# Performance work log

Hardware: AMD Instinct MI355X
Metric: run time of the kernel (lower is better)

## Reference

```python
import jax, jax.numpy as jnp
import numpy as np

FEAT = 1024
DEPTH = 3
NUM_SCALES = 5
N_NODES = 2 ** DEPTH - 1  # 7
N_LEAVES = 2 ** DEPTH     # 8
HID = 64
LN_EPS = 1e-5


def setup_inputs() -> dict:
    key = jax.random.key(0)
    ks = jax.random.split(key, 16)
    B, D = 8192, 4096
    s = 0.02
    return {
        "features": jax.random.normal(ks[0], (B, FEAT), jnp.float32),
        "logits": jax.random.normal(ks[1], (NUM_SCALES, B, D), jnp.float32),
        # all 7 tree nodes stacked (identical shapes at every level)
        "tw1": jax.random.normal(ks[2], (N_NODES, HID, FEAT), jnp.float32) * s,
        "tb1": jnp.zeros((N_NODES, HID), jnp.float32),
        "tg": jnp.ones((N_NODES, HID), jnp.float32),   # LayerNorm gamma
        "tbn": jnp.zeros((N_NODES, HID), jnp.float32),  # LayerNorm beta
        "tw2": jax.random.normal(ks[3], (N_NODES, 2, HID), jnp.float32) * s,
        "tb2": jnp.zeros((N_NODES, 2), jnp.float32),
        # leaf_to_scale: Linear(8, 10) -> GELU -> Linear(10, 5)
        "lw1": jax.random.normal(ks[4], (NUM_SCALES * 2, N_LEAVES), jnp.float32) * s,
        "lb1": jnp.zeros((NUM_SCALES * 2,), jnp.float32),
        "lw2": jax.random.normal(ks[5], (NUM_SCALES, NUM_SCALES * 2), jnp.float32) * s,
        "lb2": jnp.zeros((NUM_SCALES,), jnp.float32),
        # direct_gate: Linear(1024, 256) -> GELU -> Linear(256, 5)
        "dw1": jax.random.normal(ks[6], (FEAT // 4, FEAT), jnp.float32) * s,
        "db1": jnp.zeros((FEAT // 4,), jnp.float32),
        "dw2": jax.random.normal(ks[7], (NUM_SCALES, FEAT // 4), jnp.float32) * s,
        "db2": jnp.zeros((NUM_SCALES,), jnp.float32),
        "combine_weight": jnp.asarray(0.7, jnp.float32),
    }


def _forward(features, logits, tw1, tb1, tg, tbn, tw2, tb2,
             lw1, lb1, lw2, lb2, dw1, db1, dw2, db2, combine_weight):
    B = features.shape[0]
    # all tree nodes in one batched GEMM: [B, 7, 64]
    h = jnp.einsum("bf,nhf->bnh", features, tw1) + tb1
    mu = jnp.mean(h, axis=-1, keepdims=True)
    var = jnp.var(h, axis=-1, keepdims=True)
    h = (h - mu) / jnp.sqrt(var + LN_EPS) * tg + tbn
    h = jax.nn.gelu(h, approximate=False)  # torch GELU default = exact
    node_logits = jnp.einsum("bnh,noh->bno", h, tw2) + tb2  # [B, 7, 2]
    node_probs = jax.nn.softmax(node_logits / 0.5, axis=-1)
    # traverse levels: node ordering is BFS (level 0: node 0, level 1: 1..2, level 2: 3..6)
    p = jnp.ones((B, 1), features.dtype)
    offset = 0
    for level in range(DEPTH):
        n = 2 ** level
        pr = node_probs[:, offset:offset + n]          # [B, n, 2]
        p = (p[:, :, None] * pr).reshape(B, 2 * n)      # children interleaved L,R
        offset += n
    leaf_probs = p  # [B, 8]
    t = jax.nn.gelu(leaf_probs @ lw1.T + lb1, approximate=False)
    tree_gates = jax.nn.softmax(t @ lw2.T + lb2, axis=-1)
    d = jax.nn.gelu(features @ dw1.T + db1, approximate=False)
    direct_gates = jax.nn.softmax(d @ dw2.T + db2, axis=-1)
    w = jax.nn.sigmoid(combine_weight)
    gates = w * tree_gates + (1.0 - w) * direct_gates
    gates = gates / jnp.sum(gates, axis=-1, keepdims=True)
    # weighted combine over scales: memory-bound reduction over 5 large tensors
    combined = jnp.einsum("bs,sbd->bd", gates, logits)
    return combined, gates


def reference(features, logits, tw1, tb1, tg, tbn, tw2, tb2,
              lw1, lb1, lw2, lb2, dw1, db1, dw2, db2, combine_weight):
    return _forward(features, logits, tw1, tb1, tg, tbn, tw2, tb2,
                    lw1, lb1, lw2, lb2, dw1, db1, dw2, db2, combine_weight)
```

## Files before the change

kernel.cpp:

```cpp
#include <hip/hip_runtime.h>
#include <math.h>

#define B_SZ   8192
#define FEATN  1024
#define DCOL   4096
#define NS     5
#define NN     7
#define HIDN   64
#define NTREE  448
#define NDIR   256
#define NTOT   704

#define BM 128
#define BN 64
#define BK 16
#define LDA 132
#define LDB 68

__global__ __launch_bounds__(256) void htg_gemm(
    const float* __restrict__ A, const float* __restrict__ tw1,
    const float* __restrict__ dw1, float* __restrict__ hidden)
{
    __shared__ float As[BK * LDA];
    __shared__ float Bs[BK * LDB];
    const int tid = threadIdx.x;
    const int bm0 = blockIdx.x * BM;
    const int bn0 = blockIdx.y * BN;
    const float* Wsrc = (bn0 < NTREE) ? (tw1 + (size_t)bn0 * FEATN)
                                      : (dw1 + (size_t)(bn0 - NTREE) * FEATN);
    const int ty  = tid >> 4;
    const int tx  = tid & 15;
    const int lr  = tid >> 2;
    const int lc4 = tid & 3;

    float acc[8][4];
#pragma unroll
    for (int i = 0; i < 8; ++i)
#pragma unroll
        for (int j = 0; j < 4; ++j) acc[i][j] = 0.f;

    float4 aR0, aR1, bR;
    {
        const float* Ap = A + (size_t)(bm0 + lr) * FEATN + lc4 * 4;
        aR0 = *(const float4*)(Ap);
        aR1 = *(const float4*)(Ap + (size_t)64 * FEATN);
        bR  = *(const float4*)(Wsrc + (size_t)lr * FEATN + lc4 * 4);
    }
    const int KT = FEATN / BK;
    for (int kt = 0; kt < KT; ++kt) {
        {
            float av0[4] = {aR0.x, aR0.y, aR0.z, aR0.w};
            float av1[4] = {aR1.x, aR1.y, aR1.z, aR1.w};
            float bv[4]  = {bR.x,  bR.y,  bR.z,  bR.w};
#pragma unroll
            for (int j = 0; j < 4; ++j) {
                As[(lc4 * 4 + j) * LDA + lr]      = av0[j];
                As[(lc4 * 4 + j) * LDA + lr + 64] = av1[j];
                Bs[(lc4 * 4 + j) * LDB + lr]      = bv[j];
            }
        }
        __syncthreads();
        if (kt + 1 < KT) {
            const int k0 = (kt + 1) * BK;
            const float* Ap = A + (size_t)(bm0 + lr) * FEATN + k0 + lc4 * 4;
            aR0 = *(const float4*)(Ap);
            aR1 = *(const float4*)(Ap + (size_t)64 * FEATN);
            bR  = *(const float4*)(Wsrc + (size_t)lr * FEATN + k0 + lc4 * 4);
        }
#pragma unroll
        for (int kk = 0; kk < BK; ++kk) {
            float4 a0 = *(const float4*)&As[kk * LDA + ty * 8];
            float4 a1 = *(const float4*)&As[kk * LDA + ty * 8 + 4];
            float4 b  = *(const float4*)&Bs[kk * LDB + tx * 4];
            float av[8] = {a0.x, a0.y, a0.z, a0.w, a1.x, a1.y, a1.z, a1.w};
            float bv[4] = {b.x, b.y, b.z, b.w};
#pragma unroll
            for (int i = 0; i < 8; ++i)
#pragma unroll
                for (int j = 0; j < 4; ++j)
                    acc[i][j] = fmaf(av[i], bv[j], acc[i][j]);
        }
        __syncthreads();
    }
#pragma unroll
    for (int i = 0; i < 8; ++i) {
        const int row = bm0 + ty * 8 + i;
        float4 v = make_float4(acc[i][0], acc[i][1], acc[i][2], acc[i][3]);
        *(float4*)&hidden[(size_t)row * NTOT + bn0 + tx * 4] = v;
    }
}

__device__ inline float wredsum(float v) {
#pragma unroll
    for (int o = 32; o > 0; o >>= 1) v += __shfl_xor(v, o, 64);
    return v;
}
__device__ inline float gelu_exact(float x) {
    return 0.5f * x * (1.f + erff(x * 0.70710678118654752f));
}
__device__ inline void softmax5(float* v) {
    float m = v[0];
#pragma unroll
    for (int s = 1; s < NS; ++s) m = fmaxf(m, v[s]);
    float sum = 0.f;
#pragma unroll
    for (int s = 0; s < NS; ++s) { v[s] = expf(v[s] - m); sum += v[s]; }
    float inv = 1.f / sum;
#pragma unroll
    for (int s = 0; s < NS; ++s) v[s] *= inv;
}

__global__ __launch_bounds__(64) void htg_gates(
    const float* __restrict__ hidden,
    const float* __restrict__ tb1, const float* __restrict__ tg,
    const float* __restrict__ tbn, const float* __restrict__ tw2,
    const float* __restrict__ tb2,
    const float* __restrict__ lw1, const float* __restrict__ lb1,
    const float* __restrict__ lw2, const float* __restrict__ lb2,
    const float* __restrict__ db1, const float* __restrict__ dw2,
    const float* __restrict__ db2, const float* __restrict__ cw,
    float* __restrict__ gates_out)
{
    const int b = blockIdx.x;
    const int l = threadIdx.x;
    const float* hb = hidden + (size_t)b * NTOT;

    float np0[NN], np1[NN];
#pragma unroll
    for (int n = 0; n < NN; ++n) {
        float x  = hb[n * 64 + l] + tb1[n * 64 + l];
        float s  = wredsum(x);
        float sq = wredsum(x * x);
        float mu  = s * (1.f / 64.f);
        float var = sq * (1.f / 64.f) - mu * mu;
        float xn  = (x - mu) * rsqrtf(var + 1e-5f);
        xn = xn * tg[n * 64 + l] + tbn[n * 64 + l];
        float g = gelu_exact(xn);
        float o0 = wredsum(g * tw2[(n * 2 + 0) * 64 + l]) + tb2[n * 2 + 0];
        float o1 = wredsum(g * tw2[(n * 2 + 1) * 64 + l]) + tb2[n * 2 + 1];
        float p0 = 1.f / (1.f + expf(2.f * (o1 - o0)));
        np0[n] = p0; np1[n] = 1.f - p0;
    }
    float lp[8];
#pragma unroll
    for (int leaf = 0; leaf < 8; ++leaf) {
        const int c0 = (leaf >> 2) & 1, c1 = (leaf >> 1) & 1, c2 = leaf & 1;
        float v0 = c0 ? np1[0] : np0[0];
        float v1 = c1 ? np1[1 + c0] : np0[1 + c0];
        float v2 = c2 ? np1[3 + 2 * c0 + c1] : np0[3 + 2 * c0 + c1];
        lp[leaf] = v0 * v1 * v2;
    }
    float t[10];
#pragma unroll
    for (int j = 0; j < 10; ++j) {
        float a = lb1[j];
#pragma unroll
        for (int leaf = 0; leaf < 8; ++leaf) a = fmaf(lp[leaf], lw1[j * 8 + leaf], a);
        t[j] = gelu_exact(a);
    }
    float tgt[NS];
#pragma unroll
    for (int s = 0; s < NS; ++s) {
        float a = lb2[s];
#pragma unroll
        for (int j = 0; j < 10; ++j) a = fmaf(t[j], lw2[s * 10 + j], a);
        tgt[s] = a;
    }
    softmax5(tgt);

    float dacc[NS] = {0.f, 0.f, 0.f, 0.f, 0.f};
#pragma unroll
    for (int i = 0; i < 4; ++i) {
        const int j = i * 64 + l;
        float d = gelu_exact(hb[NTREE + j] + db1[j]);
#pragma unroll
        for (int s = 0; s < NS; ++s) dacc[s] = fmaf(d, dw2[s * 256 + j], dacc[s]);
    }
    float dgt[NS];
#pragma unroll
    for (int s = 0; s < NS; ++s) dgt[s] = wredsum(dacc[s]) + db2[s];
    softmax5(dgt);

    const float w = 1.f / (1.f + expf(-cw[0]));
    float g5[NS]; float sum = 0.f;
#pragma unroll
    for (int s = 0; s < NS; ++s) { g5[s] = w * tgt[s] + (1.f - w) * dgt[s]; sum += g5[s]; }
    float inv = 1.f / sum;
    if (l < NS) gates_out[(size_t)b * NS + l] = g5[l] * inv;
}

__global__ __launch_bounds__(256) void htg_combine(
    const float* __restrict__ logits, const float* __restrict__ gates,
    float* __restrict__ out)
{
    const int b  = blockIdx.x >> 2;
    const int d4 = ((blockIdx.x & 3) << 8) + threadIdx.x;
    float g[NS];
#pragma unroll
    for (int s = 0; s < NS; ++s) g[s] = gates[(size_t)b * NS + s];
    const float4* lp = (const float4*)logits;
    const size_t base = (size_t)b * (DCOL / 4) + d4;
    float4 a = make_float4(0.f, 0.f, 0.f, 0.f);
#pragma unroll
    for (int s = 0; s < NS; ++s) {
        float4 v = lp[(size_t)s * B_SZ * (DCOL / 4) + base];
        a.x = fmaf(g[s], v.x, a.x);
        a.y = fmaf(g[s], v.y, a.y);
        a.z = fmaf(g[s], v.z, a.z);
        a.w = fmaf(g[s], v.w, a.w);
    }
    ((float4*)out)[base] = a;
}

extern "C" void kernel_launch(void* const* d_in, const int* in_sizes, int n_in,
                              void* d_out, int out_size, void* d_ws, size_t ws_size,
                              hipStream_t stream) {
    const float* features = (const float*)d_in[0];
    const float* logits   = (const float*)d_in[1];
    const float* tw1      = (const float*)d_in[2];
    const float* tb1      = (const float*)d_in[3];
    const float* tg       = (const float*)d_in[4];
    const float* tbn      = (const float*)d_in[5];
    const float* tw2      = (const float*)d_in[6];
    const float* tb2      = (const float*)d_in[7];
    const float* lw1      = (const float*)d_in[8];
    const float* lb1      = (const float*)d_in[9];
    const float* lw2      = (const float*)d_in[10];
    const float* lb2      = (const float*)d_in[11];
    const float* dw1      = (const float*)d_in[12];
    const float* db1      = (const float*)d_in[13];
    const float* dw2      = (const float*)d_in[14];
    const float* db2      = (const float*)d_in[15];
    const float* cw       = (const float*)d_in[16];

    float* out = (float*)d_out;
    float* gates = out + (size_t)B_SZ * DCOL;

    const size_t hidden_bytes = (size_t)B_SZ * NTOT * sizeof(float);
    float* hidden = (ws_size >= hidden_bytes) ? (float*)d_ws : (float*)d_out;

    dim3 gemm_grid(B_SZ / BM, NTOT / BN);
    htg_gemm<<<gemm_grid, 256, 0, stream>>>(features, tw1, dw1, hidden);

    htg_gates<<<B_SZ, 64, 0, stream>>>(hidden, tb1, tg, tbn, tw2, tb2,
                                       lw1, lb1, lw2, lb2, db1, dw2, db2, cw,
                                       gates);

    htg_combine<<<B_SZ * 4, 256, 0, stream>>>(logits, gates, out);
}
```

Measured before the change: 1.095 ms.

## Fuse LayerNorm/GELU/node heads into GEMM epilogue and slim gate kernel

The GEMM epilogue now applies bias, LayerNorm, exact GELU and the two-output node head per 64-column tile. For the direct branch it applies GELU and partial dot products with dw2. Only 7 node probabilities and 20 partial sums per row are written, instead of the full 704-wide hidden matrix. The gate kernel becomes one thread per row reading that small scratch. The combine kernel handles one row per block with nontemporal loads and stores. This removes a large intermediate round trip and the per-row wave reductions, at the cost of more epilogue work and register pressure in the GEMM.

```diff
diff --git a/kernel.cpp b/kernel.cpp
--- a/kernel.cpp
+++ b/kernel.cpp
@@ -11,15 +11,27 @@
 #define NDIR   256
 #define NTOT   704
 
+
 #define BM 128
 #define BN 64
 #define BK 16
 #define LDA 132
 #define LDB 68
 
-__global__ __launch_bounds__(256) void htg_gemm(
+typedef float f32x4_t __attribute__((ext_vector_type(4)));
+
+__device__ inline float gelu_exact(float x) {
+    return 0.5f * x * (1.f + erff(x * 0.70710678118654752f));
+}
+
+__global__ __launch_bounds__(256) void htg_gemm_fused(
     const float* __restrict__ A, const float* __restrict__ tw1,
-    const float* __restrict__ dw1, float* __restrict__ hidden)
+    const float* __restrict__ dw1,
+    const float* __restrict__ tb1, const float* __restrict__ tg,
+    const float* __restrict__ tbn, const float* __restrict__ tw2,
+    const float* __restrict__ tb2,
+    const float* __restrict__ db1, const float* __restrict__ dw2,
+    float* __restrict__ np_out, float* __restrict__ dpart_out)
 {
     __shared__ float As[BK * LDA];
     __shared__ float Bs[BK * LDB];
@@ -82,22 +94,89 @@
         }
         __syncthreads();
     }
-#pragma unroll
-    for (int i = 0; i < 8; ++i) {
-        const int row = bm0 + ty * 8 + i;
-        float4 v = make_float4(acc[i][0], acc[i][1], acc[i][2], acc[i][3]);
-        *(float4*)&hidden[(size_t)row * NTOT + bn0 + tx * 4] = v;
-    }
-}
-
-__device__ inline float wredsum(float v) {
-#pragma unroll
-    for (int o = 32; o > 0; o >>= 1) v += __shfl_xor(v, o, 64);
-    return v;
-}
-__device__ inline float gelu_exact(float x) {
-    return 0.5f * x * (1.f + erff(x * 0.70710678118654752f));
-}
+
+    const int ib = blockIdx.y;
+    if (ib < NN) {
+        const int n = ib;
+        const int col = tx * 4;
+        const float4 tb1v = *(const float4*)&tb1[n * HIDN + col];
+        const float4 tgv  = *(const float4*)&tg [n * HIDN + col];
+        const float4 tbnv = *(const float4*)&tbn[n * HIDN + col];
+        const float4 w2av = *(const float4*)&tw2[(n * 2 + 0) * HIDN + col];
+        const float4 w2bv = *(const float4*)&tw2[(n * 2 + 1) * HIDN + col];
+        const float b2a = tb2[n * 2], b2b = tb2[n * 2 + 1];
+        const float tb1a[4] = {tb1v.x, tb1v.y, tb1v.z, tb1v.w};
+        const float tga[4]  = {tgv.x,  tgv.y,  tgv.z,  tgv.w};
+        const float tbna[4] = {tbnv.x, tbnv.y, tbnv.z, tbnv.w};
+        const float w2aa[4] = {w2av.x, w2av.y, w2av.z, w2av.w};
+        const float w2ba[4] = {w2bv.x, w2bv.y, w2bv.z, w2bv.w};
+#pragma unroll
+        for (int i = 0; i < 8; ++i) {
+            float x[4]; float s = 0.f, sq = 0.f;
+#pragma unroll
+            for (int j = 0; j < 4; ++j) {
+                x[j] = acc[i][j] + tb1a[j];
+                s += x[j];
+                sq = fmaf(x[j], x[j], sq);
+            }
+#pragma unroll
+            for (int o = 8; o > 0; o >>= 1) {
+                s  += __shfl_xor(s,  o, 64);
+                sq += __shfl_xor(sq, o, 64);
+            }
+            const float mu  = s * (1.f / 64.f);
+            const float var = sq * (1.f / 64.f) - mu * mu;
+            const float rs  = rsqrtf(var + 1e-5f);
+            float o0 = 0.f, o1 = 0.f;
+#pragma unroll
+            for (int j = 0; j < 4; ++j) {
+                const float g = gelu_exact((x[j] - mu) * rs * tga[j] + tbna[j]);
+                o0 = fmaf(g, w2aa[j], o0);
+                o1 = fmaf(g, w2ba[j], o1);
+            }
+#pragma unroll
+            for (int o = 8; o > 0; o >>= 1) {
+                o0 += __shfl_xor(o0, o, 64);
+                o1 += __shfl_xor(o1, o, 64);
+            }
+            o0 += b2a; o1 += b2b;
+            const float p0 = 1.f / (1.f + expf(2.f * (o1 - o0)));
+            if (tx == 0) np_out[(size_t)(bm0 + ty * 8 + i) * NN + n] = p0;
+        }
+    } else {
+        const int cb  = ib - NN;
+        const int col = cb * HIDN + tx * 4;
+        const float4 dbv = *(const float4*)&db1[col];
+        const float dba[4] = {dbv.x, dbv.y, dbv.z, dbv.w};
+        float w2[NS][4];
+#pragma unroll
+        for (int s5 = 0; s5 < NS; ++s5) {
+            const float4 v = *(const float4*)&dw2[s5 * NDIR + col];
+            w2[s5][0] = v.x; w2[s5][1] = v.y; w2[s5][2] = v.z; w2[s5][3] = v.w;
+        }
+#pragma unroll
+        for (int i = 0; i < 8; ++i) {
+            float part[NS] = {0.f, 0.f, 0.f, 0.f, 0.f};
+#pragma unroll
+            for (int j = 0; j < 4; ++j) {
+                const float d = gelu_exact(acc[i][j] + dba[j]);
+#pragma unroll
+                for (int s5 = 0; s5 < NS; ++s5) part[s5] = fmaf(d, w2[s5][j], part[s5]);
+            }
+#pragma unroll
+            for (int o = 8; o > 0; o >>= 1)
+#pragma unroll
+                for (int s5 = 0; s5 < NS; ++s5) part[s5] += __shfl_xor(part[s5], o, 64);
+            if (tx == 0) {
+                const size_t r = bm0 + ty * 8 + i;
+#pragma unroll
+                for (int s5 = 0; s5 < NS; ++s5)
+                    dpart_out[r * 20 + cb * NS + s5] = part[s5];
+            }
+        }
+    }
+}
+
 __device__ inline void softmax5(float* v) {
     float m = v[0];
 #pragma unroll
@@ -105,49 +184,32 @@
     float sum = 0.f;
 #pragma unroll
     for (int s = 0; s < NS; ++s) { v[s] = expf(v[s] - m); sum += v[s]; }
-    float inv = 1.f / sum;
+    const float inv = 1.f / sum;
 #pragma unroll
     for (int s = 0; s < NS; ++s) v[s] *= inv;
 }
 
-__global__ __launch_bounds__(64) void htg_gates(
-    const float* __restrict__ hidden,
-    const float* __restrict__ tb1, const float* __restrict__ tg,
-    const float* __restrict__ tbn, const float* __restrict__ tw2,
-    const float* __restrict__ tb2,
+__global__ __launch_bounds__(256) void htg_gates_lite(
+    const float* __restrict__ np, const float* __restrict__ dpart,
     const float* __restrict__ lw1, const float* __restrict__ lb1,
     const float* __restrict__ lw2, const float* __restrict__ lb2,
-    const float* __restrict__ db1, const float* __restrict__ dw2,
     const float* __restrict__ db2, const float* __restrict__ cw,
     float* __restrict__ gates_out)
 {
-    const int b = blockIdx.x;
-    const int l = threadIdx.x;
-    const float* hb = hidden + (size_t)b * NTOT;
-
+    const int b = blockIdx.x * 256 + threadIdx.x;
     float np0[NN], np1[NN];
 #pragma unroll
     for (int n = 0; n < NN; ++n) {
-        float x  = hb[n * 64 + l] + tb1[n * 64 + l];
-        float s  = wredsum(x);
-        float sq = wredsum(x * x);
-        float mu  = s * (1.f / 64.f);
-        float var = sq * (1.f / 64.f) - mu * mu;
-        float xn  = (x - mu) * rsqrtf(var + 1e-5f);
-        xn = xn * tg[n * 64 + l] + tbn[n * 64 + l];
-        float g = gelu_exact(xn);
-        float o0 = wredsum(g * tw2[(n * 2 + 0) * 64 + l]) + tb2[n * 2 + 0];
-        float o1 = wredsum(g * tw2[(n * 2 + 1) * 64 + l]) + tb2[n * 2 + 1];
-        float p0 = 1.f / (1.f + expf(2.f * (o1 - o0)));
-        np0[n] = p0; np1[n] = 1.f - p0;
+        np0[n] = np[(size_t)b * NN + n];
+        np1[n] = 1.f - np0[n];
     }
     float lp[8];
 #pragma unroll
     for (int leaf = 0; leaf < 8; ++leaf) {
         const int c0 = (leaf >> 2) & 1, c1 = (leaf >> 1) & 1, c2 = leaf & 1;
-        float v0 = c0 ? np1[0] : np0[0];
-        float v1 = c1 ? np1[1 + c0] : np0[1 + c0];
-        float v2 = c2 ? np1[3 + 2 * c0 + c1] : np0[3 + 2 * c0 + c1];
+        const float v0 = c0 ? np1[0] : np0[0];
+        const float v1 = c1 ? np1[1 + c0] : np0[1 + c0];
+        const float v2 = c2 ? np1[3 + 2 * c0 + c1] : np0[3 + 2 * c0 + c1];
         lp[leaf] = v0 * v1 * v2;
     }
     float t[10];
@@ -167,49 +229,52 @@
         tgt[s] = a;
     }
     softmax5(tgt);
-
-    float dacc[NS] = {0.f, 0.f, 0.f, 0.f, 0.f};
-#pragma unroll
-    for (int i = 0; i < 4; ++i) {
-        const int j = i * 64 + l;
-        float d = gelu_exact(hb[NTREE + j] + db1[j]);
-#pragma unroll
-        for (int s = 0; s < NS; ++s) dacc[s] = fmaf(d, dw2[s * 256 + j], dacc[s]);
-    }
     float dgt[NS];
 #pragma unroll
-    for (int s = 0; s < NS; ++s) dgt[s] = wredsum(dacc[s]) + db2[s];
+    for (int s = 0; s < NS; ++s) {
+        float a = db2[s];
+#pragma unroll
+        for (int cb = 0; cb < 4; ++cb) a += dpart[(size_t)b * 20 + cb * NS + s];
+        dgt[s] = a;
+    }
     softmax5(dgt);
-
     const float w = 1.f / (1.f + expf(-cw[0]));
     float g5[NS]; float sum = 0.f;
 #pragma unroll
-    for (int s = 0; s < NS; ++s) { g5[s] = w * tgt[s] + (1.f - w) * dgt[s]; sum += g5[s]; }
-    float inv = 1.f / sum;
-    if (l < NS) gates_out[(size_t)b * NS + l] = g5[l] * inv;
+    for (int s = 0; s < NS; ++s) {
+        g5[s] = fmaf(w, tgt[s] - dgt[s], dgt[s]);
+        sum += g5[s];
+    }
+    const float inv = 1.f / sum;
+#pragma unroll
+    for (int s = 0; s < NS; ++s) gates_out[(size_t)b * NS + s] = g5[s] * inv;
 }
 
 __global__ __launch_bounds__(256) void htg_combine(
     const float* __restrict__ logits, const float* __restrict__ gates,
     float* __restrict__ out)
 {
-    const int b  = blockIdx.x >> 2;
-    const int d4 = ((blockIdx.x & 3) << 8) + threadIdx.x;
+    const int b = blockIdx.x;
     float g[NS];
 #pragma unroll
     for (int s = 0; s < NS; ++s) g[s] = gates[(size_t)b * NS + s];
-    const float4* lp = (const float4*)logits;
-    const size_t base = (size_t)b * (DCOL / 4) + d4;
-    float4 a = make_float4(0.f, 0.f, 0.f, 0.f);
-#pragma unroll
-    for (int s = 0; s < NS; ++s) {
-        float4 v = lp[(size_t)s * B_SZ * (DCOL / 4) + base];
-        a.x = fmaf(g[s], v.x, a.x);
-        a.y = fmaf(g[s], v.y, a.y);
-        a.z = fmaf(g[s], v.z, a.z);
-        a.w = fmaf(g[s], v.w, a.w);
-    }
-    ((float4*)out)[base] = a;
+    const f32x4_t* lp = (const f32x4_t*)logits;
+    f32x4_t* op = (f32x4_t*)out;
+    const size_t rowbase = (size_t)b * (DCOL / 4);
+#pragma unroll
+    for (int u = 0; u < 4; ++u) {
+        const size_t idx = rowbase + u * 256 + threadIdx.x;
+        f32x4_t a = (f32x4_t)(0.f);
+#pragma unroll
+        for (int s = 0; s < NS; ++s) {
+            const f32x4_t v = __builtin_nontemporal_load(&lp[(size_t)s * B_SZ * (DCOL / 4) + idx]);
+            a.x = fmaf(g[s], v.x, a.x);
+            a.y = fmaf(g[s], v.y, a.y);
+            a.z = fmaf(g[s], v.z, a.z);
+            a.w = fmaf(g[s], v.w, a.w);
+        }
+        __builtin_nontemporal_store(a, &op[idx]);
+    }
 }
 
 extern "C" void kernel_launch(void* const* d_in, const int* in_sizes, int n_in,
@@ -233,18 +298,22 @@
     const float* db2      = (const float*)d_in[15];
     const float* cw       = (const float*)d_in[16];
 
-    float* out = (float*)d_out;
+    float* out   = (float*)d_out;
     float* gates = out + (size_t)B_SZ * DCOL;
 
-    const size_t hidden_bytes = (size_t)B_SZ * NTOT * sizeof(float);
-    float* hidden = (ws_size >= hidden_bytes) ? (float*)d_ws : (float*)d_out;
+    const size_t scratch_bytes = (size_t)B_SZ * 27 * sizeof(float);
+    float* scratch   = (ws_size >= scratch_bytes) ? (float*)d_ws : (float*)d_out;
+    float* np_buf    = scratch;
+    float* dpart_buf = scratch + (size_t)B_SZ * NN;
 
     dim3 gemm_grid(B_SZ / BM, NTOT / BN);
-    htg_gemm<<<gemm_grid, 256, 0, stream>>>(features, tw1, dw1, hidden);
-
-    htg_gates<<<B_SZ, 64, 0, stream>>>(hidden, tb1, tg, tbn, tw2, tb2,
-                                       lw1, lb1, lw2, lb2, db1, dw2, db2, cw,
-                                       gates);
-
-    htg_combine<<<B_SZ * 4, 256, 0, stream>>>(logits, gates, out);
-}
+    htg_gemm_fused<<<gemm_grid, 256, 0, stream>>>(features, tw1, dw1,
+                                                  tb1, tg, tbn, tw2, tb2,
+                                                  db1, dw2, np_buf, dpart_buf);
+
+    htg_gates_lite<<<B_SZ / 256, 256, 0, stream>>>(np_buf, dpart_buf,
+                                                   lw1, lb1, lw2, lb2, db2, cw,
+                                                   gates);
+
+    htg_combine<<<B_SZ, 256, 0, stream>>>(logits, gates, out);
+}
```

Result: faster. 1.059 ms (-3.3%).
